# Kernel optimization log

Hardware: AMD Instinct MI355X
Metric: run time of the kernel (lower is better)

Reference implementation:

```python
import jax, jax.numpy as jnp
import numpy as np

B, N, F = 32, 512, 128
AGG, FCH, NCLS, NLAYER = 128, 256, 10, 3


def setup_inputs() -> dict:
    key = jax.random.key(0)
    ks = jax.random.split(key, 10)
    s = 1.0 / np.sqrt(F)
    inp = {
        "x": jax.random.normal(ks[0], (B, N, F), jnp.float32),
        "L_re": jax.random.normal(ks[1], (B, N, N), jnp.float32) / np.sqrt(N),
        "L_im": jax.random.normal(ks[2], (B, N, N), jnp.float32) / np.sqrt(N),
        # stacked complex layer weights (layer0: F->AGG, rest AGG->AGG; F==AGG)
        "Wr": jax.random.normal(ks[3], (NLAYER, F, AGG), jnp.float32) * s,
        "Wi": jax.random.normal(ks[4], (NLAYER, F, AGG), jnp.float32) * s,
        "fc1_w": jax.random.normal(ks[5], (FCH, 2 * AGG), jnp.float32) / np.sqrt(2 * AGG),
        "fc1_b": jnp.zeros((FCH,), jnp.float32),
        "fc2_w": jax.random.normal(ks[6], (NCLS, FCH), jnp.float32) / np.sqrt(FCH),
        "fc2_b": jnp.zeros((NCLS,), jnp.float32),
    }
    return inp


def reference(x, L_re, L_im, Wr, Wi, fc1_w, fc1_b, fc2_w, fc2_b):
    L = jax.lax.complex(L_re, L_im)                      # [B,N,N] complex magnetic Laplacian
    h = x.astype(jnp.complex64)                          # x + 0j, [B,N,F]
    for i in range(NLAYER):
        W = jax.lax.complex(Wr[i], Wi[i])                # [F,AGG] complex
        h = jnp.einsum('bnm,bmf->bnf', L, h)             # complex aggregation
        h = jnp.einsum('bnf,fo->bno', h, W)              # complex transform
        # complex ReLU: keep z where Re(z) >= 0, else 0 (vectorized mask-multiply)
        h = jnp.where(jnp.real(h) >= 0, h, jnp.zeros((), h.dtype))
        # dropout skipped (eval mode)
    # readout: mean over nodes, concat real & imag -> [B, 2*AGG]
    p = jnp.mean(h, axis=1)
    feat = jnp.concatenate([jnp.real(p), jnp.imag(p)], axis=-1)
    z = jax.nn.relu(feat @ fc1_w.T + fc1_b)
    logits = z @ fc2_w.T + fc2_b
    return jax.nn.softmax(logits, axis=-1)
```

## Files before the change

kernel.cpp:

```cpp
#include <hip/hip_runtime.h>
#include <hip/hip_bf16.h>
#include <math.h>

#define B_SZ   32
#define N_SZ   512
#define F_SZ   128

typedef __attribute__((ext_vector_type(8))) short short8v;
typedef __attribute__((ext_vector_type(4))) short short4v;
typedef __attribute__((ext_vector_type(4))) float f32x4;

typedef const __attribute__((address_space(1))) unsigned int* gas1_t;
typedef __attribute__((address_space(3))) unsigned int* las3_t;
#define GLD16(gsrc, ldst) __builtin_amdgcn_global_load_lds( \
    (gas1_t)(const void*)(gsrc), (las3_t)(unsigned int)(size_t)(void*)(ldst), 16, 0, 0)

#define MFMA16(a, bb, c) __builtin_amdgcn_mfma_f32_16x16x32_bf16((a), (bb), (c), 0, 0, 0)

__device__ __forceinline__ short bfh(float v) {
    __hip_bfloat16 h = __float2bfloat16(v);
    return __builtin_bit_cast(short, h);
}
__device__ __forceinline__ float bf2f(short s) {
    unsigned u = ((unsigned)(unsigned short)s) << 16;
    return __builtin_bit_cast(float, u);
}
__device__ __forceinline__ void split1(float v, short& h, short& l) {
    short hs = bfh(v);
    h = hs;
    l = bfh(v - bf2f(hs));
}
__device__ __forceinline__ void splitpack(const float4& a, const float4& b,
                                          short8v& h, short8v& l) {
    const float va[8] = {a.x, a.y, a.z, a.w, b.x, b.y, b.z, b.w};
    #pragma unroll
    for (int j = 0; j < 8; ++j) {
        short hs, ls;
        split1(va[j], hs, ls);
        h[j] = hs; l[j] = ls;
    }
}

template<int HAS_BIM>
__global__ __launch_bounds__(256, 2)
void fused_layer(const float* __restrict__ Lre, const float* __restrict__ Lim,
                 const short* __restrict__ Brh, const short* __restrict__ Brl,
                 const short* __restrict__ Bih, const short* __restrict__ Bil,
                 const short* __restrict__ Wrh, const short* __restrict__ Wrl,
                 const short* __restrict__ Wih, const short* __restrict__ Wil,
                 short* __restrict__ Orh, short* __restrict__ Orl,
                 short* __restrict__ Oih, short* __restrict__ Oil)
{
    __shared__ __align__(16) char ldsraw[65536];
    short (*Bs)[4][4096] = (short(*)[4][4096])ldsraw;
    short (*Ts)[32 * 136] = (short(*)[32 * 136])ldsraw;

    const int t = threadIdx.x;
    const int lid = blockIdx.y * 16 + blockIdx.x;
    const int nl = (lid & 7) * 64 + (lid >> 3);
    const int b = nl >> 4;
    const int rowBase = (nl & 15) * 32;

    const float* pLre = Lre + (long)b * (N_SZ * N_SZ);
    const float* pLim = Lim + (long)b * (N_SZ * N_SZ);
    const long sB = (long)F_SZ * N_SZ;
    const short* pBrh = Brh + (long)b * sB;
    const short* pBrl = Brl + (long)b * sB;
    const short* pBih = HAS_BIM ? (Bih + (long)b * sB) : nullptr;
    const short* pBil = HAS_BIM ? (Bil + (long)b * sB) : nullptr;

    const int wn = t >> 6;
    const int l = t & 63;
    const int r16 = l & 15, g = l >> 4;

    short8v SGN;
    #pragma unroll
    for (int j = 0; j < 8; ++j) SGN[j] = (short)0x8000;

    const f32x4 z4 = {0.f, 0.f, 0.f, 0.f};
    f32x4 accR[2][2], accI[2][2];
    #pragma unroll
    for (int i = 0; i < 2; ++i)
        #pragma unroll
        for (int j = 0; j < 2; ++j) { accR[i][j] = z4; accI[i][j] = z4; }

#define STAGE_B(buf, kb)                                                     \
    {                                                                        \
        _Pragma("unroll")                                                    \
        for (int rep = 0; rep < 2; ++rep) {                                  \
            const int i_ = t + rep * 256;                                    \
            const int n_ = i_ >> 2, s_ = i_ & 3;                             \
            const int c_ = s_ ^ ((n_ >> 1) & 3);                             \
            const long so_ = (long)n_ * 512 + (kb) + 8 * c_;                 \
            GLD16(pBrh + so_, &Bs[buf][0][i_ * 8]);                          \
            GLD16(pBrl + so_, &Bs[buf][1][i_ * 8]);                          \
            if (HAS_BIM) {                                                   \
                GLD16(pBih + so_, &Bs[buf][2][i_ * 8]);                      \
                GLD16(pBil + so_, &Bs[buf][3][i_ * 8]);                      \
            }                                                                \
        }                                                                    \
    }

#define LOAD_A(R, kb)                                                        \
    {                                                                        \
        _Pragma("unroll")                                                    \
        for (int tm_ = 0; tm_ < 2; ++tm_) {                                  \
            const long ro_ = (long)(rowBase + tm_ * 16 + r16) * 512 + (kb) + g * 8; \
            R[tm_][0][0] = *(const float4*)(pLre + ro_);                     \
            R[tm_][0][1] = *(const float4*)(pLre + ro_ + 4);                 \
            R[tm_][1][0] = *(const float4*)(pLim + ro_);                     \
            R[tm_][1][1] = *(const float4*)(pLim + ro_ + 4);                 \
        }                                                                    \
    }

#define STEP(buf, R)                                                         \
    {                                                                        \
        short8v FA[2][4];                                                    \
        _Pragma("unroll")                                                    \
        for (int tm_ = 0; tm_ < 2; ++tm_) {                                  \
            splitpack(R[tm_][0][0], R[tm_][0][1], FA[tm_][0], FA[tm_][1]);   \
            splitpack(R[tm_][1][0], R[tm_][1][1], FA[tm_][2], FA[tm_][3]);   \
        }                                                                    \
        short8v fB[2][4];                                                    \
        _Pragma("unroll")                                                    \
        for (int tn_ = 0; tn_ < 2; ++tn_) {                                  \
            const int n_ = wn * 32 + tn_ * 16 + r16;                         \
            const int off_ = n_ * 32 + 8 * (g ^ ((n_ >> 1) & 3));            \
            fB[tn_][0] = *(const short8v*)&Bs[buf][0][off_];                 \
            fB[tn_][1] = *(const short8v*)&Bs[buf][1][off_];                 \
            if (HAS_BIM) {                                                   \
                fB[tn_][2] = *(const short8v*)&Bs[buf][2][off_];             \
                fB[tn_][3] = *(const short8v*)&Bs[buf][3][off_];             \
            }                                                                \
        }                                                                    \
        _Pragma("unroll")                                                    \
        for (int tm_ = 0; tm_ < 2; ++tm_) {                                  \
            const short8v nIh_ = FA[tm_][2] ^ SGN;                           \
            const short8v nIl_ = FA[tm_][3] ^ SGN;                           \
            _Pragma("unroll")                                                \
            for (int tn_ = 0; tn_ < 2; ++tn_) {                              \
                accR[tm_][tn_] = MFMA16(FA[tm_][0], fB[tn_][0], accR[tm_][tn_]); \
                accR[tm_][tn_] = MFMA16(FA[tm_][1], fB[tn_][0], accR[tm_][tn_]); \
                accR[tm_][tn_] = MFMA16(FA[tm_][0], fB[tn_][1], accR[tm_][tn_]); \
                accI[tm_][tn_] = MFMA16(FA[tm_][2], fB[tn_][0], accI[tm_][tn_]); \
                accI[tm_][tn_] = MFMA16(FA[tm_][3], fB[tn_][0], accI[tm_][tn_]); \
                accI[tm_][tn_] = MFMA16(FA[tm_][2], fB[tn_][1], accI[tm_][tn_]); \
                if (HAS_BIM) {                                               \
                    accR[tm_][tn_] = MFMA16(nIh_, fB[tn_][2], accR[tm_][tn_]);   \
                    accR[tm_][tn_] = MFMA16(nIl_, fB[tn_][2], accR[tm_][tn_]);   \
                    accR[tm_][tn_] = MFMA16(nIh_, fB[tn_][3], accR[tm_][tn_]);   \
                    accI[tm_][tn_] = MFMA16(FA[tm_][0], fB[tn_][2], accI[tm_][tn_]); \
                    accI[tm_][tn_] = MFMA16(FA[tm_][1], fB[tn_][2], accI[tm_][tn_]); \
                    accI[tm_][tn_] = MFMA16(FA[tm_][0], fB[tn_][3], accI[tm_][tn_]); \
                }                                                            \
            }                                                                \
        }                                                                    \
    }

    float4 Ra[2][2][2], Rb[2][2][2];
    STAGE_B(0, 0);
    LOAD_A(Ra, 0);
    __syncthreads();

    for (int k2 = 0; k2 < 8; ++k2) {
        const int kb = k2 * 64;
        STAGE_B(1, kb + 32);
        LOAD_A(Rb, kb + 32);
        STEP(0, Ra);
        __syncthreads();
        if (k2 < 7) {
            STAGE_B(0, kb + 64);
            LOAD_A(Ra, kb + 64);
        }
        STEP(1, Rb);
        __syncthreads();
    }

    #pragma unroll
    for (int tm = 0; tm < 2; ++tm)
        #pragma unroll
        for (int tn = 0; tn < 2; ++tn) {
            const int f = wn * 32 + tn * 16 + r16;
            #pragma unroll
            for (int rr = 0; rr < 4; ++rr) {
                const int node = tm * 16 + 4 * g + rr;
                short hs, ls;
                split1(accR[tm][tn][rr], hs, ls);
                Ts[0][node * 136 + f] = hs; Ts[1][node * 136 + f] = ls;
                split1(accI[tm][tn][rr], hs, ls);
                Ts[2][node * 136 + f] = hs; Ts[3][node * 136 + f] = ls;
            }
        }
    __syncthreads();

    f32x4 acc2R[2][2], acc2I[2][2];
    #pragma unroll
    for (int i = 0; i < 2; ++i)
        #pragma unroll
        for (int j = 0; j < 2; ++j) { acc2R[i][j] = z4; acc2I[i][j] = z4; }

    #pragma unroll
    for (int c = 0; c < 4; ++c) {
        short8v fW[2][4];
        #pragma unroll
        for (int tn = 0; tn < 2; ++tn) {
            const long wo = (long)(wn * 32 + tn * 16 + r16) * 128 + c * 32 + g * 8;
            fW[tn][0] = *(const short8v*)(Wrh + wo);
            fW[tn][1] = *(const short8v*)(Wrl + wo);
            fW[tn][2] = *(const short8v*)(Wih + wo);
            fW[tn][3] = *(const short8v*)(Wil + wo);
        }
        short8v fT[2][4];
        #pragma unroll
        for (int tm = 0; tm < 2; ++tm) {
            const int off = (tm * 16 + r16) * 136 + c * 32 + g * 8;
            #pragma unroll
            for (int p = 0; p < 4; ++p)
                fT[tm][p] = *(const short8v*)&Ts[p][off];
        }
        #pragma unroll
        for (int tm = 0; tm < 2; ++tm) {
            const short8v nIh = fT[tm][2] ^ SGN;
            const short8v nIl = fT[tm][3] ^ SGN;
            #pragma unroll
            for (int tn = 0; tn < 2; ++tn) {
                acc2R[tm][tn] = MFMA16(fT[tm][0], fW[tn][0], acc2R[tm][tn]);
                acc2R[tm][tn] = MFMA16(fT[tm][1], fW[tn][0], acc2R[tm][tn]);
                acc2R[tm][tn] = MFMA16(fT[tm][0], fW[tn][1], acc2R[tm][tn]);
                acc2R[tm][tn] = MFMA16(nIh, fW[tn][2], acc2R[tm][tn]);
                acc2R[tm][tn] = MFMA16(nIl, fW[tn][2], acc2R[tm][tn]);
                acc2R[tm][tn] = MFMA16(nIh, fW[tn][3], acc2R[tm][tn]);
                acc2I[tm][tn] = MFMA16(fT[tm][2], fW[tn][0], acc2I[tm][tn]);
                acc2I[tm][tn] = MFMA16(fT[tm][3], fW[tn][0], acc2I[tm][tn]);
                acc2I[tm][tn] = MFMA16(fT[tm][2], fW[tn][1], acc2I[tm][tn]);
                acc2I[tm][tn] = MFMA16(fT[tm][0], fW[tn][2], acc2I[tm][tn]);
                acc2I[tm][tn] = MFMA16(fT[tm][1], fW[tn][2], acc2I[tm][tn]);
                acc2I[tm][tn] = MFMA16(fT[tm][0], fW[tn][3], acc2I[tm][tn]);
            }
        }
    }

    #pragma unroll
    for (int tm = 0; tm < 2; ++tm)
        #pragma unroll
        for (int tn = 0; tn < 2; ++tn) {
            const int out = wn * 32 + tn * 16 + r16;
            const int node0 = rowBase + tm * 16 + 4 * g;
            short4v rh, rl, ih, il;
            #pragma unroll
            for (int rr = 0; rr < 4; ++rr) {
                float cr = acc2R[tm][tn][rr], ci = acc2I[tm][tn][rr];
                if (cr < 0.f) { cr = 0.f; ci = 0.f; }
                short hs, ls;
                split1(cr, hs, ls); rh[rr] = hs; rl[rr] = ls;
                split1(ci, hs, ls); ih[rr] = hs; il[rr] = ls;
            }
            const long base = ((long)b * 128 + out) * 512 + node0;
            *(short4v*)(Orh + base) = rh;
            *(short4v*)(Orl + base) = rl;
            *(short4v*)(Oih + base) = ih;
            *(short4v*)(Oil + base) = il;
        }
#undef STAGE_B
#undef LOAD_A
#undef STEP
}

__global__ __launch_bounds__(256)
void split_x_kernel(const float* __restrict__ x, short* __restrict__ Xh,
                    short* __restrict__ Xl)
{
    __shared__ float XT[128][65];
    const int b = blockIdx.x >> 3, nc = blockIdx.x & 7;
    const int t = threadIdx.x;
    {
        const int nlan = t & 63, fc = t >> 6;
        const float* src = x + ((long)b * 512 + nc * 64 + nlan) * 128 + fc * 32;
        #pragma unroll
        for (int q = 0; q < 8; ++q) {
            float4 v = *(const float4*)(src + q * 4);
            XT[fc * 32 + q * 4 + 0][nlan] = v.x;
            XT[fc * 32 + q * 4 + 1][nlan] = v.y;
            XT[fc * 32 + q * 4 + 2][nlan] = v.z;
            XT[fc * 32 + q * 4 + 3][nlan] = v.w;
        }
    }
    __syncthreads();
    const int f = t >> 1, half = t & 1;
    short8v H[4], L[4];
    #pragma unroll
    for (int i = 0; i < 32; ++i) {
        short hs, ls;
        split1(XT[f][half * 32 + i], hs, ls);
        H[i >> 3][i & 7] = hs;
        L[i >> 3][i & 7] = ls;
    }
    const long base = ((long)b * 128 + f) * 512 + nc * 64 + half * 32;
    #pragma unroll
    for (int q = 0; q < 4; ++q) {
        *(short8v*)(Xh + base + q * 8) = H[q];
        *(short8v*)(Xl + base + q * 8) = L[q];
    }
}

__global__ __launch_bounds__(128)
void split_w_kernel(const float* __restrict__ Wr, const float* __restrict__ Wi,
                    short* __restrict__ Wrh, short* __restrict__ Wrl,
                    short* __restrict__ Wih, short* __restrict__ Wil)
{
    const int layer = blockIdx.x >> 7, n = blockIdx.x & 127;
    const int k = threadIdx.x;
    const long src = ((long)layer * 128 + k) * 128 + n;
    const long dst = ((long)layer * 128 + n) * 128 + k;
    short hs, ls;
    split1(Wr[src], hs, ls); Wrh[dst] = hs; Wrl[dst] = ls;
    split1(Wi[src], hs, ls); Wih[dst] = hs; Wil[dst] = ls;
}

__global__ __launch_bounds__(256)
void readout_kernel(const short* __restrict__ Hrh, const short* __restrict__ Hrl,
                    const short* __restrict__ Hih, const short* __restrict__ Hil,
                    float* __restrict__ part)
{
    const int b = blockIdx.x >> 3, nc = blockIdx.x & 7;
    const int t = threadIdx.x;
    const int f = t & 127;
    const short* Ph = (t < 128) ? Hrh : Hih;
    const short* Pl = (t < 128) ? Hrl : Hil;
    const long base = ((long)b * 128 + f) * 512 + nc * 64;
    float s = 0.f;
    #pragma unroll
    for (int q = 0; q < 8; ++q) {
        short8v vh = *(const short8v*)(Ph + base + q * 8);
        short8v vl = *(const short8v*)(Pl + base + q * 8);
        #pragma unroll
        for (int j = 0; j < 8; ++j) s += bf2f(vh[j]) + bf2f(vl[j]);
    }
    part[((long)b * 8 + nc) * 256 + t] = s;
}

__global__ __launch_bounds__(256)
void head_kernel(const float* __restrict__ part,
                 const float* __restrict__ w1, const float* __restrict__ b1,
                 const float* __restrict__ w2, const float* __restrict__ b2,
                 float* __restrict__ out)
{
    __shared__ float sf[256];
    __shared__ float sz[256];
    __shared__ float sl[16];
    const int b = blockIdx.x;
    const int t = threadIdx.x;

    float s = 0.f;
    #pragma unroll
    for (int nc = 0; nc < 8; ++nc) s += part[((long)b * 8 + nc) * 256 + t];
    sf[t] = s * (1.0f / 512.0f);
    __syncthreads();

    float acc = b1[t];
    const float* wrow = w1 + (long)t * 256;
    #pragma unroll 8
    for (int j = 0; j < 256; ++j) acc = fmaf(sf[j], wrow[j], acc);
    sz[t] = fmaxf(acc, 0.f);
    __syncthreads();

    if (t < 10) {
        float lg = b2[t];
        const float* w2r = w2 + (long)t * 256;
        #pragma unroll 8
        for (int j = 0; j < 256; ++j) lg = fmaf(sz[j], w2r[j], lg);
        sl[t] = lg;
    }
    __syncthreads();
    if (t == 0) {
        float m = sl[0];
        for (int c = 1; c < 10; ++c) m = fmaxf(m, sl[c]);
        float e[10]; float ss = 0.f;
        for (int c = 0; c < 10; ++c) { e[c] = expf(sl[c] - m); ss += e[c]; }
        const float inv = 1.f / ss;
        for (int c = 0; c < 10; ++c) out[b * 10 + c] = e[c] * inv;
    }
}

extern "C" void kernel_launch(void* const* d_in, const int* in_sizes, int n_in,
                              void* d_out, int out_size, void* d_ws, size_t ws_size,
                              hipStream_t stream)
{
    const float* x     = (const float*)d_in[0];
    const float* Lre   = (const float*)d_in[1];
    const float* Lim   = (const float*)d_in[2];
    const float* Wr    = (const float*)d_in[3];
    const float* Wi    = (const float*)d_in[4];
    const float* fc1_w = (const float*)d_in[5];
    const float* fc1_b = (const float*)d_in[6];
    const float* fc2_w = (const float*)d_in[7];
    const float* fc2_b = (const float*)d_in[8];
    float* out = (float*)d_out;

    const long BNF = (long)B_SZ * N_SZ * F_SZ;
    short* h0 = (short*)d_ws;
    short* h1 = h0 + 4 * BNF;
    short* Wrh = h1 + 4 * BNF;
    short* Wrl = Wrh + 3 * 128 * 128;
    short* Wih = Wrl + 3 * 128 * 128;
    short* Wil = Wih + 3 * 128 * 128;
    float* part = (float*)(Wil + 3 * 128 * 128);

    const dim3 ggrid(16, 32);
    const long wsz = 128 * 128;

    split_w_kernel<<<384, 128, 0, stream>>>(Wr, Wi, Wrh, Wrl, Wih, Wil);
    split_x_kernel<<<256, 256, 0, stream>>>(x, h0, h0 + BNF);

    fused_layer<0><<<ggrid, 256, 0, stream>>>(
        Lre, Lim, h0, h0 + BNF, nullptr, nullptr,
        Wrh, Wrl, Wih, Wil,
        h1, h1 + BNF, h1 + 2 * BNF, h1 + 3 * BNF);
    fused_layer<1><<<ggrid, 256, 0, stream>>>(
        Lre, Lim, h1, h1 + BNF, h1 + 2 * BNF, h1 + 3 * BNF,
        Wrh + wsz, Wrl + wsz, Wih + wsz, Wil + wsz,
        h0, h0 + BNF, h0 + 2 * BNF, h0 + 3 * BNF);
    fused_layer<1><<<ggrid, 256, 0, stream>>>(
        Lre, Lim, h0, h0 + BNF, h0 + 2 * BNF, h0 + 3 * BNF,
        Wrh + 2 * wsz, Wrl + 2 * wsz, Wih + 2 * wsz, Wil + 2 * wsz,
        h1, h1 + BNF, h1 + 2 * BNF, h1 + 3 * BNF);

    readout_kernel<<<256, 256, 0, stream>>>(
        h1, h1 + BNF, h1 + 2 * BNF, h1 + 3 * BNF, part);
    head_kernel<<<32, 256, 0, stream>>>(part, fc1_w, fc1_b, fc2_w, fc2_b, out);
}
```

Measured before the change: 302.4 us.

## Drop LDS staging for direct loads, fuse readout into last layer, merge prep kernels

The aggregation GEMM no longer stages the bf16 hidden state through double-buffered LDS with global_load_lds. Each wave now reads its B fragments directly from global memory inside a simple unrolled loop. The last layer reduces its ReLU outputs to per-row-block partial sums in place of writing H, which removes the separate readout kernel. The x and W split kernels are merged into one launch. The risks are losing the explicit prefetch overlap and adding redundant global reads of B across waves.

```diff
diff --git a/kernel.cpp b/kernel.cpp
--- a/kernel.cpp
+++ b/kernel.cpp
@@ -9,11 +9,6 @@
 typedef __attribute__((ext_vector_type(8))) short short8v;
 typedef __attribute__((ext_vector_type(4))) short short4v;
 typedef __attribute__((ext_vector_type(4))) float f32x4;
-
-typedef const __attribute__((address_space(1))) unsigned int* gas1_t;
-typedef __attribute__((address_space(3))) unsigned int* las3_t;
-#define GLD16(gsrc, ldst) __builtin_amdgcn_global_load_lds( \
-    (gas1_t)(const void*)(gsrc), (las3_t)(unsigned int)(size_t)(void*)(ldst), 16, 0, 0)
 
 #define MFMA16(a, bb, c) __builtin_amdgcn_mfma_f32_16x16x32_bf16((a), (bb), (c), 0, 0, 0)
 
@@ -41,7 +36,7 @@
     }
 }
 
-template<int HAS_BIM>
+template<int HAS_BIM, int LAST>
 __global__ __launch_bounds__(256, 2)
 void fused_layer(const float* __restrict__ Lre, const float* __restrict__ Lim,
                  const short* __restrict__ Brh, const short* __restrict__ Brl,
@@ -49,17 +44,17 @@
                  const short* __restrict__ Wrh, const short* __restrict__ Wrl,
                  const short* __restrict__ Wih, const short* __restrict__ Wil,
                  short* __restrict__ Orh, short* __restrict__ Orl,
-                 short* __restrict__ Oih, short* __restrict__ Oil)
+                 short* __restrict__ Oih, short* __restrict__ Oil,
+                 float* __restrict__ part)
 {
-    __shared__ __align__(16) char ldsraw[65536];
-    short (*Bs)[4][4096] = (short(*)[4][4096])ldsraw;
-    short (*Ts)[32 * 136] = (short(*)[32 * 136])ldsraw;
+    __shared__ short Ts[4][32 * 136];
 
     const int t = threadIdx.x;
-    const int lid = blockIdx.y * 16 + blockIdx.x;
+    const int lid = blockIdx.x;
     const int nl = (lid & 7) * 64 + (lid >> 3);
     const int b = nl >> 4;
-    const int rowBase = (nl & 15) * 32;
+    const int rb = nl & 15;
+    const int rowBase = rb * 32;
 
     const float* pLre = Lre + (long)b * (N_SZ * N_SZ);
     const float* pLim = Lim + (long)b * (N_SZ * N_SZ);
@@ -84,96 +79,65 @@
         #pragma unroll
         for (int j = 0; j < 2; ++j) { accR[i][j] = z4; accI[i][j] = z4; }
 
-#define STAGE_B(buf, kb)                                                     \
-    {                                                                        \
-        _Pragma("unroll")                                                    \
-        for (int rep = 0; rep < 2; ++rep) {                                  \
-            const int i_ = t + rep * 256;                                    \
-            const int n_ = i_ >> 2, s_ = i_ & 3;                             \
-            const int c_ = s_ ^ ((n_ >> 1) & 3);                             \
-            const long so_ = (long)n_ * 512 + (kb) + 8 * c_;                 \
-            GLD16(pBrh + so_, &Bs[buf][0][i_ * 8]);                          \
-            GLD16(pBrl + so_, &Bs[buf][1][i_ * 8]);                          \
-            if (HAS_BIM) {                                                   \
-                GLD16(pBih + so_, &Bs[buf][2][i_ * 8]);                      \
-                GLD16(pBil + so_, &Bs[buf][3][i_ * 8]);                      \
-            }                                                                \
-        }                                                                    \
-    }
-
-#define LOAD_A(R, kb)                                                        \
-    {                                                                        \
-        _Pragma("unroll")                                                    \
-        for (int tm_ = 0; tm_ < 2; ++tm_) {                                  \
-            const long ro_ = (long)(rowBase + tm_ * 16 + r16) * 512 + (kb) + g * 8; \
-            R[tm_][0][0] = *(const float4*)(pLre + ro_);                     \
-            R[tm_][0][1] = *(const float4*)(pLre + ro_ + 4);                 \
-            R[tm_][1][0] = *(const float4*)(pLim + ro_);                     \
-            R[tm_][1][1] = *(const float4*)(pLim + ro_ + 4);                 \
-        }                                                                    \
-    }
-
-#define STEP(buf, R)                                                         \
-    {                                                                        \
-        short8v FA[2][4];                                                    \
-        _Pragma("unroll")                                                    \
-        for (int tm_ = 0; tm_ < 2; ++tm_) {                                  \
-            splitpack(R[tm_][0][0], R[tm_][0][1], FA[tm_][0], FA[tm_][1]);   \
-            splitpack(R[tm_][1][0], R[tm_][1][1], FA[tm_][2], FA[tm_][3]);   \
-        }                                                                    \
-        short8v fB[2][4];                                                    \
-        _Pragma("unroll")                                                    \
-        for (int tn_ = 0; tn_ < 2; ++tn_) {                                  \
-            const int n_ = wn * 32 + tn_ * 16 + r16;                         \
-            const int off_ = n_ * 32 + 8 * (g ^ ((n_ >> 1) & 3));            \
-            fB[tn_][0] = *(const short8v*)&Bs[buf][0][off_];                 \
-            fB[tn_][1] = *(const short8v*)&Bs[buf][1][off_];                 \
-            if (HAS_BIM) {                                                   \
-                fB[tn_][2] = *(const short8v*)&Bs[buf][2][off_];             \
-                fB[tn_][3] = *(const short8v*)&Bs[buf][3][off_];             \
-            }                                                                \
-        }                                                                    \
-        _Pragma("unroll")                                                    \
-        for (int tm_ = 0; tm_ < 2; ++tm_) {                                  \
-            const short8v nIh_ = FA[tm_][2] ^ SGN;                           \
-            const short8v nIl_ = FA[tm_][3] ^ SGN;                           \
-            _Pragma("unroll")                                                \
-            for (int tn_ = 0; tn_ < 2; ++tn_) {                              \
-                accR[tm_][tn_] = MFMA16(FA[tm_][0], fB[tn_][0], accR[tm_][tn_]); \
-                accR[tm_][tn_] = MFMA16(FA[tm_][1], fB[tn_][0], accR[tm_][tn_]); \
-                accR[tm_][tn_] = MFMA16(FA[tm_][0], fB[tn_][1], accR[tm_][tn_]); \
-                accI[tm_][tn_] = MFMA16(FA[tm_][2], fB[tn_][0], accI[tm_][tn_]); \
-                accI[tm_][tn_] = MFMA16(FA[tm_][3], fB[tn_][0], accI[tm_][tn_]); \
-                accI[tm_][tn_] = MFMA16(FA[tm_][2], fB[tn_][1], accI[tm_][tn_]); \
-                if (HAS_BIM) {                                               \
-                    accR[tm_][tn_] = MFMA16(nIh_, fB[tn_][2], accR[tm_][tn_]);   \
-                    accR[tm_][tn_] = MFMA16(nIl_, fB[tn_][2], accR[tm_][tn_]);   \
-                    accR[tm_][tn_] = MFMA16(nIh_, fB[tn_][3], accR[tm_][tn_]);   \
-                    accI[tm_][tn_] = MFMA16(FA[tm_][0], fB[tn_][2], accI[tm_][tn_]); \
-                    accI[tm_][tn_] = MFMA16(FA[tm_][1], fB[tn_][2], accI[tm_][tn_]); \
-                    accI[tm_][tn_] = MFMA16(FA[tm_][0], fB[tn_][3], accI[tm_][tn_]); \
-                }                                                            \
-            }                                                                \
-        }                                                                    \
-    }
-
-    float4 Ra[2][2][2], Rb[2][2][2];
-    STAGE_B(0, 0);
-    LOAD_A(Ra, 0);
-    __syncthreads();
-
-    for (int k2 = 0; k2 < 8; ++k2) {
-        const int kb = k2 * 64;
-        STAGE_B(1, kb + 32);
-        LOAD_A(Rb, kb + 32);
-        STEP(0, Ra);
-        __syncthreads();
-        if (k2 < 7) {
-            STAGE_B(0, kb + 64);
-            LOAD_A(Ra, kb + 64);
-        }
-        STEP(1, Rb);
-        __syncthreads();
+    const long aro0 = (long)(rowBase + r16) * 512 + g * 8;
+    const long aro1 = (long)(rowBase + 16 + r16) * 512 + g * 8;
+    const long bro0 = (long)(wn * 32 + r16) * 512 + g * 8;
+    const long bro1 = (long)(wn * 32 + 16 + r16) * 512 + g * 8;
+
+    #pragma unroll 2
+    for (int kb = 0; kb < 512; kb += 32) {
+        short8v fB[2][4];
+        {
+            const long bo0 = bro0 + kb, bo1 = bro1 + kb;
+            fB[0][0] = *(const short8v*)(pBrh + bo0);
+            fB[1][0] = *(const short8v*)(pBrh + bo1);
+            fB[0][1] = *(const short8v*)(pBrl + bo0);
+            fB[1][1] = *(const short8v*)(pBrl + bo1);
+            if (HAS_BIM) {
+                fB[0][2] = *(const short8v*)(pBih + bo0);
+                fB[1][2] = *(const short8v*)(pBih + bo1);
+                fB[0][3] = *(const short8v*)(pBil + bo0);
+                fB[1][3] = *(const short8v*)(pBil + bo1);
+            }
+        }
+        short8v FA[2][4];
+        {
+            const long ao0 = aro0 + kb, ao1 = aro1 + kb;
+            float4 x0 = *(const float4*)(pLre + ao0);
+            float4 x1 = *(const float4*)(pLre + ao0 + 4);
+            float4 y0 = *(const float4*)(pLim + ao0);
+            float4 y1 = *(const float4*)(pLim + ao0 + 4);
+            splitpack(x0, x1, FA[0][0], FA[0][1]);
+            splitpack(y0, y1, FA[0][2], FA[0][3]);
+            x0 = *(const float4*)(pLre + ao1);
+            x1 = *(const float4*)(pLre + ao1 + 4);
+            y0 = *(const float4*)(pLim + ao1);
+            y1 = *(const float4*)(pLim + ao1 + 4);
+            splitpack(x0, x1, FA[1][0], FA[1][1]);
+            splitpack(y0, y1, FA[1][2], FA[1][3]);
+        }
+        #pragma unroll
+        for (int tm = 0; tm < 2; ++tm) {
+            const short8v nIh = FA[tm][2] ^ SGN;
+            const short8v nIl = FA[tm][3] ^ SGN;
+            #pragma unroll
+            for (int tn = 0; tn < 2; ++tn) {
+                accR[tm][tn] = MFMA16(FA[tm][0], fB[tn][0], accR[tm][tn]);
+                accR[tm][tn] = MFMA16(FA[tm][1], fB[tn][0], accR[tm][tn]);
+                accR[tm][tn] = MFMA16(FA[tm][0], fB[tn][1], accR[tm][tn]);
+                accI[tm][tn] = MFMA16(FA[tm][2], fB[tn][0], accI[tm][tn]);
+                accI[tm][tn] = MFMA16(FA[tm][3], fB[tn][0], accI[tm][tn]);
+                accI[tm][tn] = MFMA16(FA[tm][2], fB[tn][1], accI[tm][tn]);
+                if (HAS_BIM) {
+                    accR[tm][tn] = MFMA16(nIh, fB[tn][2], accR[tm][tn]);
+                    accR[tm][tn] = MFMA16(nIl, fB[tn][2], accR[tm][tn]);
+                    accR[tm][tn] = MFMA16(nIh, fB[tn][3], accR[tm][tn]);
+                    accI[tm][tn] = MFMA16(FA[tm][0], fB[tn][2], accI[tm][tn]);
+                    accI[tm][tn] = MFMA16(FA[tm][1], fB[tn][2], accI[tm][tn]);
+                    accI[tm][tn] = MFMA16(FA[tm][0], fB[tn][3], accI[tm][tn]);
+                }
+            }
+        }
     }
 
     #pragma unroll
@@ -240,103 +204,102 @@
         }
     }
 
-    #pragma unroll
-    for (int tm = 0; tm < 2; ++tm)
+    if (LAST) {
         #pragma unroll
         for (int tn = 0; tn < 2; ++tn) {
-            const int out = wn * 32 + tn * 16 + r16;
-            const int node0 = rowBase + tm * 16 + 4 * g;
-            short4v rh, rl, ih, il;
-            #pragma unroll
-            for (int rr = 0; rr < 4; ++rr) {
-                float cr = acc2R[tm][tn][rr], ci = acc2I[tm][tn][rr];
-                if (cr < 0.f) { cr = 0.f; ci = 0.f; }
-                short hs, ls;
-                split1(cr, hs, ls); rh[rr] = hs; rl[rr] = ls;
-                split1(ci, hs, ls); ih[rr] = hs; il[rr] = ls;
-            }
-            const long base = ((long)b * 128 + out) * 512 + node0;
-            *(short4v*)(Orh + base) = rh;
-            *(short4v*)(Orl + base) = rl;
-            *(short4v*)(Oih + base) = ih;
-            *(short4v*)(Oil + base) = il;
-        }
-#undef STAGE_B
-#undef LOAD_A
-#undef STEP
+            float sR = 0.f, sI = 0.f;
+            #pragma unroll
+            for (int tm = 0; tm < 2; ++tm)
+                #pragma unroll
+                for (int rr = 0; rr < 4; ++rr) {
+                    float cr = acc2R[tm][tn][rr], ci = acc2I[tm][tn][rr];
+                    if (cr < 0.f) { cr = 0.f; ci = 0.f; }
+                    sR += cr; sI += ci;
+                }
+            sR += __shfl_xor(sR, 16); sR += __shfl_xor(sR, 32);
+            sI += __shfl_xor(sI, 16); sI += __shfl_xor(sI, 32);
+            if (g == 0) {
+                const int f = wn * 32 + tn * 16 + r16;
+                float* pp = part + ((long)b * 16 + rb) * 256;
+                pp[f] = sR;
+                pp[128 + f] = sI;
+            }
+        }
+    } else {
+        #pragma unroll
+        for (int tm = 0; tm < 2; ++tm)
+            #pragma unroll
+            for (int tn = 0; tn < 2; ++tn) {
+                const int out = wn * 32 + tn * 16 + r16;
+                const int node0 = rowBase + tm * 16 + 4 * g;
+                short4v rh, rl, ih, il;
+                #pragma unroll
+                for (int rr = 0; rr < 4; ++rr) {
+                    float cr = acc2R[tm][tn][rr], ci = acc2I[tm][tn][rr];
+                    if (cr < 0.f) { cr = 0.f; ci = 0.f; }
+                    short hs, ls;
+                    split1(cr, hs, ls); rh[rr] = hs; rl[rr] = ls;
+                    split1(ci, hs, ls); ih[rr] = hs; il[rr] = ls;
+                }
+                const long base = ((long)b * 128 + out) * 512 + node0;
+                *(short4v*)(Orh + base) = rh;
+                *(short4v*)(Orl + base) = rl;
+                *(short4v*)(Oih + base) = ih;
+                *(short4v*)(Oil + base) = il;
+            }
+    }
 }
 
 __global__ __launch_bounds__(256)
-void split_x_kernel(const float* __restrict__ x, short* __restrict__ Xh,
-                    short* __restrict__ Xl)
+void prep_kernel(const float* __restrict__ x,
+                 const float* __restrict__ Wr, const float* __restrict__ Wi,
+                 short* __restrict__ Xh, short* __restrict__ Xl,
+                 short* __restrict__ Wrh, short* __restrict__ Wrl,
+                 short* __restrict__ Wih, short* __restrict__ Wil)
 {
-    __shared__ float XT[128][65];
-    const int b = blockIdx.x >> 3, nc = blockIdx.x & 7;
     const int t = threadIdx.x;
-    {
-        const int nlan = t & 63, fc = t >> 6;
-        const float* src = x + ((long)b * 512 + nc * 64 + nlan) * 128 + fc * 32;
-        #pragma unroll
-        for (int q = 0; q < 8; ++q) {
-            float4 v = *(const float4*)(src + q * 4);
-            XT[fc * 32 + q * 4 + 0][nlan] = v.x;
-            XT[fc * 32 + q * 4 + 1][nlan] = v.y;
-            XT[fc * 32 + q * 4 + 2][nlan] = v.z;
-            XT[fc * 32 + q * 4 + 3][nlan] = v.w;
-        }
-    }
-    __syncthreads();
-    const int f = t >> 1, half = t & 1;
-    short8v H[4], L[4];
-    #pragma unroll
-    for (int i = 0; i < 32; ++i) {
+    if (blockIdx.x < 256) {
+        __shared__ float XT[128][65];
+        const int b = blockIdx.x >> 3, nc = blockIdx.x & 7;
+        {
+            const int nlan = t & 63, fc = t >> 6;
+            const float* src = x + ((long)b * 512 + nc * 64 + nlan) * 128 + fc * 32;
+            #pragma unroll
+            for (int q = 0; q < 8; ++q) {
+                float4 v = *(const float4*)(src + q * 4);
+                XT[fc * 32 + q * 4 + 0][nlan] = v.x;
+                XT[fc * 32 + q * 4 + 1][nlan] = v.y;
+                XT[fc * 32 + q * 4 + 2][nlan] = v.z;
+                XT[fc * 32 + q * 4 + 3][nlan] = v.w;
+            }
+        }
+        __syncthreads();
+        const int f = t >> 1, half = t & 1;
+        short8v H[4], L[4];
+        #pragma unroll
+        for (int i = 0; i < 32; ++i) {
+            short hs, ls;
+            split1(XT[f][half * 32 + i], hs, ls);
+            H[i >> 3][i & 7] = hs;
+            L[i >> 3][i & 7] = ls;
+        }
+        const long base = ((long)b * 128 + f) * 512 + nc * 64 + half * 32;
+        #pragma unroll
+        for (int q = 0; q < 4; ++q) {
+            *(short8v*)(Xh + base + q * 8) = H[q];
+            *(short8v*)(Xl + base + q * 8) = L[q];
+        }
+    } else {
+        const int idx = (blockIdx.x - 256) * 256 + t;
+        const int layer = idx >> 14;
+        const int rem = idx & 16383;
+        const int n = rem >> 7, k = rem & 127;
+        const long src = ((long)layer * 128 + k) * 128 + n;
+        const long dst = ((long)layer * 128 + n) * 128 + k;
         short hs, ls;
-        split1(XT[f][half * 32 + i], hs, ls);
-        H[i >> 3][i & 7] = hs;
-        L[i >> 3][i & 7] = ls;
-    }
-    const long base = ((long)b * 128 + f) * 512 + nc * 64 + half * 32;
-    #pragma unroll
-    for (int q = 0; q < 4; ++q) {
-        *(short8v*)(Xh + base + q * 8) = H[q];
-        *(short8v*)(Xl + base + q * 8) = L[q];
-    }
-}
-
-__global__ __launch_bounds__(128)
-void split_w_kernel(const float* __restrict__ Wr, const float* __restrict__ Wi,
-                    short* __restrict__ Wrh, short* __restrict__ Wrl,
-                    short* __restrict__ Wih, short* __restrict__ Wil)
-{
-    const int layer = blockIdx.x >> 7, n = blockIdx.x & 127;
-    const int k = threadIdx.x;
-    const long src = ((long)layer * 128 + k) * 128 + n;
-    const long dst = ((long)layer * 128 + n) * 128 + k;
-    short hs, ls;
-    split1(Wr[src], hs, ls); Wrh[dst] = hs; Wrl[dst] = ls;
-    split1(Wi[src], hs, ls); Wih[dst] = hs; Wil[dst] = ls;
-}
-
-__global__ __launch_bounds__(256)
-void readout_kernel(const short* __restrict__ Hrh, const short* __restrict__ Hrl,
-                    const short* __restrict__ Hih, const short* __restrict__ Hil,
-                    float* __restrict__ part)
-{
-    const int b = blockIdx.x >> 3, nc = blockIdx.x & 7;
-    const int t = threadIdx.x;
-    const int f = t & 127;
-    const short* Ph = (t < 128) ? Hrh : Hih;
-    const short* Pl = (t < 128) ? Hrl : Hil;
-    const long base = ((long)b * 128 + f) * 512 + nc * 64;
-    float s = 0.f;
-    #pragma unroll
-    for (int q = 0; q < 8; ++q) {
-        short8v vh = *(const short8v*)(Ph + base + q * 8);
-        short8v vl = *(const short8v*)(Pl + base + q * 8);
-        #pragma unroll
-        for (int j = 0; j < 8; ++j) s += bf2f(vh[j]) + bf2f(vl[j]);
-    }
-    part[((long)b * 8 + nc) * 256 + t] = s;
+        split1(Wr[src], hs, ls); Wrh[dst] = hs; Wrl[dst] = ls;
+        split1(Wi[src], hs, ls); Wih[dst] = hs; Wil[dst] = ls;
+    }
 }
 
 __global__ __launch_bounds__(256)
@@ -353,7 +316,8 @@
 
     float s = 0.f;
     #pragma unroll
-    for (int nc = 0; nc < 8; ++nc) s += part[((long)b * 8 + nc) * 256 + t];
+    for (int rbk = 0; rbk < 16; ++rbk)
+        s += part[((long)b * 16 + rbk) * 256 + t];
     sf[t] = s * (1.0f / 512.0f);
     __syncthreads();
 
@@ -406,26 +370,23 @@
     short* Wil = Wih + 3 * 128 * 128;
     float* part = (float*)(Wil + 3 * 128 * 128);
 
-    const dim3 ggrid(16, 32);
     const long wsz = 128 * 128;
 
-    split_w_kernel<<<384, 128, 0, stream>>>(Wr, Wi, Wrh, Wrl, Wih, Wil);
-    split_x_kernel<<<256, 256, 0, stream>>>(x, h0, h0 + BNF);
-
-    fused_layer<0><<<ggrid, 256, 0, stream>>>(
+    prep_kernel<<<448, 256, 0, stream>>>(x, Wr, Wi, h0, h0 + BNF,
+                                         Wrh, Wrl, Wih, Wil);
+
+    fused_layer<0, 0><<<512, 256, 0, stream>>>(
         Lre, Lim, h0, h0 + BNF, nullptr, nullptr,
         Wrh, Wrl, Wih, Wil,
-        h1, h1 + BNF, h1 + 2 * BNF, h1 + 3 * BNF);
-    fused_layer<1><<<ggrid, 256, 0, stream>>>(
+        h1, h1 + BNF, h1 + 2 * BNF, h1 + 3 * BNF, nullptr);
+    fused_layer<1, 0><<<512, 256, 0, stream>>>(
         Lre, Lim, h1, h1 + BNF, h1 + 2 * BNF, h1 + 3 * BNF,
         Wrh + wsz, Wrl + wsz, Wih + wsz, Wil + wsz,
-        h0, h0 + BNF, h0 + 2 * BNF, h0 + 3 * BNF);
-    fused_layer<1><<<ggrid, 256, 0, stream>>>(
+        h0, h0 + BNF, h0 + 2 * BNF, h0 + 3 * BNF, nullptr);
+    fused_layer<1, 1><<<512, 256, 0, stream>>>(
         Lre, Lim, h0, h0 + BNF, h0 + 2 * BNF, h0 + 3 * BNF,
         Wrh + 2 * wsz, Wrl + 2 * wsz, Wih + 2 * wsz, Wil + 2 * wsz,
-        h1, h1 + BNF, h1 + 2 * BNF, h1 + 3 * BNF);
-
-    readout_kernel<<<256, 256, 0, stream>>>(
-        h1, h1 + BNF, h1 + 2 * BNF, h1 + 3 * BNF, part);
-    head_kernel<<<32, 256, 0, stream>>>(part, fc1_w, fc1_b, fc2_w, fc2_b, out);
-}
+        nullptr, nullptr, nullptr, nullptr, part);
+
+    head_kernel<<<B_SZ, 256, 0, stream>>>(part, fc1_w, fc1_b, fc2_w, fc2_b, out);
+}
```

Measured after the change: 326.1 us. +7.8%, slower.
